# Optimization experiments

Hardware: AMD Instinct MI355X
Metric: run time of the kernel (lower is better)

## Reference

```python
import jax, jax.numpy as jnp
import numpy as np

N_USER = 50000
N_ITEM = 30000
NNZ = 500000  # user-item interactions; edges duplicated symmetrically -> E = 2*NNZ
EMB = 64
N_LAYERS = 2
N_FACTORS = 4
N_ITERATIONS = 2


def setup_inputs() -> dict:
    key = jax.random.key(0)
    k1, k2, k3, k4 = jax.random.split(key, 4)
    user_emb = jax.random.normal(k1, (N_USER, EMB), dtype=jnp.float32) * 0.1
    item_emb = jax.random.normal(k2, (N_ITEM, EMB), dtype=jnp.float32) * 0.1
    row = jax.random.randint(k3, (NNZ,), 0, N_USER, dtype=jnp.int32)
    col = jax.random.randint(k4, (NNZ,), 0, N_ITEM, dtype=jnp.int32) + N_USER
    # symmetric edge list exactly as the torch module builds it
    all_h_list = jnp.concatenate([row, col], axis=0)
    all_t_list = jnp.concatenate([col, row], axis=0)
    return {"user_emb": user_emb, "item_emb": item_emb,
            "all_h_list": all_h_list, "all_t_list": all_t_list}


def _dgcf_forward(user_emb, item_emb, all_h_list, all_t_list):
    n_user = user_emb.shape[0]
    ego = jnp.concatenate([user_emb, item_emb], axis=0)  # [N, D]
    N, D = ego.shape
    F = N_FACTORS
    d = D // F
    E = all_h_list.shape[0]
    dtype = ego.dtype

    all_embeddings = [ego]
    A = jnp.ones((E, F), dtype=dtype)  # A_values init

    for _layer in range(N_LAYERS):
        # torch.chunk along dim 1 == reshape [N, F, d]
        chunks = ego.reshape(N, F, d)
        tail_chunks = chunks[all_t_list]  # [E, F, d] gather of tail embeddings
        factor_emb = None
        for _t in range(N_ITERATIONS):
            # build_matrix, vectorized over the F factors
            normA = jax.nn.softmax(A, axis=1)                        # [E, F]
            dval = jax.ops.segment_sum(normA, all_h_list, num_segments=N)  # [N, F]
            dinv = 1.0 / jnp.sqrt(jnp.clip(dval, 1e-8))
            edge_weight = normA * dinv[all_h_list] * dinv[all_t_list]  # [E, F]
            # message passing per factor: gather tail, weight, scatter to head
            edge_val = tail_chunks * edge_weight[:, :, None]           # [E, F, d]
            factor_emb = jax.ops.segment_sum(edge_val, all_h_list, num_segments=N)  # [N, F, d]
            # dynamic routing update of A
            head = factor_emb[all_h_list]                              # [E, F, d]
            head = head / jnp.clip(jnp.linalg.norm(head, axis=-1, keepdims=True), 1e-12)
            tail = tail_chunks / jnp.clip(jnp.linalg.norm(tail_chunks, axis=-1, keepdims=True), 1e-12)
            A_iter = jnp.sum(head * jnp.tanh(tail), axis=-1)           # [E, F]
            A = A + A_iter
        ego = factor_emb.reshape(N, D)  # concat of factor chunks (last iteration)
        all_embeddings.append(ego)

    all_emb = jnp.mean(jnp.stack(all_embeddings, axis=1), axis=1)  # [N, D]
    return all_emb[:n_user], all_emb[n_user:]


def reference(user_emb, item_emb, all_h_list, all_t_list):
    return _dgcf_forward(user_emb, item_emb, all_h_list, all_t_list)
```

## Files before the change

kernel.cpp:

```cpp
#include <hip/hip_runtime.h>
#include <hip/hip_bf16.h>

#define N_USER 50000
#define N_ITEM 30000
#define NTOT   80000
#define EMB    64
#define FAC    4
#define EDGES  1000000
#define LOG4   1.3862943611198906f
#define SB     1024
#define NBLK   79
#define NBUCK  512
#define BBLK   512
#define BCH    1954


__device__ inline float bf2f(unsigned short u) {
    return __uint_as_float(((unsigned int)u) << 16);
}
__device__ inline unsigned short f2bf(float f) {
    unsigned int x = __float_as_uint(f);
    x += 0x7FFFu + ((x >> 16) & 1u);
    return (unsigned short)(x >> 16);
}
__device__ inline float dot2(unsigned int a, unsigned int b) {
    float a0 = __uint_as_float(a << 16), a1 = __uint_as_float(a & 0xFFFF0000u);
    float b0 = __uint_as_float(b << 16), b1 = __uint_as_float(b & 0xFFFF0000u);
    return a0 * b0 + a1 * b1;
}
__device__ inline int bucket_of(int h) { return (int)(((unsigned)h * NBUCK) / (unsigned)NTOT); }
__device__ inline int bucket_lo(int k) { return (k * NTOT + NBUCK - 1) / NBUCK; }

__global__ void k_detect(const unsigned short* __restrict__ raw, int* __restrict__ flag) {
    __shared__ int s;
    if (threadIdx.x == 0) s = 0;
    __syncthreads();
    int c = 0;
    for (int i = threadIdx.x; i < 16384; i += 256) {
        unsigned short u = raw[i];
        if ((u & 0x7F80) == 0x7F80) c++;
    }
    atomicAdd(&s, c);
    __syncthreads();
    if (threadIdx.x == 0) *flag = (s > 0) ? 1 : 0;
}

__global__ void k_init(const void* __restrict__ ue, const void* __restrict__ ie,
                       const int* __restrict__ flag,
                       unsigned short* __restrict__ egoh,
                       unsigned short* __restrict__ tnh0) {
    int gid = blockIdx.x * blockDim.x + threadIdx.x;
    int wid = gid >> 6;
    int lane = threadIdx.x & 63;
    if (wid >= NTOT) return;
    int i = wid * 64 + lane;
    bool isf32 = (*flag != 0);
    float v;
    if (i < N_USER * EMB) {
        v = isf32 ? ((const float*)ue)[i]
                  : __bfloat162float(((const __hip_bfloat16*)ue)[i]);
    } else {
        int j = i - N_USER * EMB;
        v = isf32 ? ((const float*)ie)[j]
                  : __bfloat162float(((const __hip_bfloat16*)ie)[j]);
    }
    egoh[i] = f2bf(v);
    float ss = v * v;
    ss += __shfl_xor(ss, 1); ss += __shfl_xor(ss, 2);
    ss += __shfl_xor(ss, 4); ss += __shfl_xor(ss, 8);
    float rr = 1.0f / fmaxf(sqrtf(ss), 1e-12f);
    tnh0[i] = f2bf(tanhf(v * rr));
}

__global__ void k_deg(const int* __restrict__ h, int* __restrict__ deg) {
    int e = blockIdx.x * blockDim.x + threadIdx.x;
    if (e < EDGES) atomicAdd(&deg[h[e]], 1);
}

__global__ void k_scan1(const int* __restrict__ deg, int* __restrict__ off,
                        int* __restrict__ bsum) {
    __shared__ int buf[SB];
    int tid = threadIdx.x;
    int i = blockIdx.x * SB + tid;
    int v = (i < NTOT) ? deg[i] : 0;
    buf[tid] = v;
    __syncthreads();
    for (int s = 1; s < SB; s <<= 1) {
        int t = (tid >= s) ? buf[tid - s] : 0;
        __syncthreads();
        buf[tid] += t;
        __syncthreads();
    }
    if (i < NTOT) off[i] = buf[tid] - v;
    if (tid == SB - 1) bsum[blockIdx.x] = buf[tid];
}

__global__ void k_scan2(const int* __restrict__ bsum, int* __restrict__ bbase) {
    __shared__ int b[128];
    int tid = threadIdx.x;
    int v = (tid < NBLK) ? bsum[tid] : 0;
    b[tid] = v;
    __syncthreads();
    for (int s = 1; s < 128; s <<= 1) {
        int t = (tid >= s) ? b[tid - s] : 0;
        __syncthreads();
        b[tid] += t;
        __syncthreads();
    }
    if (tid < NBLK) bbase[tid] = b[tid] - v;
}

__global__ void k_scan3(int* __restrict__ off, const int* __restrict__ bbase,
                        const int* __restrict__ deg, float* __restrict__ dvacc) {
    int i = blockIdx.x * blockDim.x + threadIdx.x;
    if (i < NTOT) {
        off[i] = off[i] + bbase[i >> 10];
        float d = 0.25f * (float)deg[i];
        ((float4*)dvacc)[i] = make_float4(d, d, d, d);
    }
    if (i == 0) off[NTOT] = EDGES;
}

__global__ void k_bcnt(const int* __restrict__ hl, int* __restrict__ cnt) {
    __shared__ int hist[NBUCK];
    int b = blockIdx.x, tid = threadIdx.x;
    for (int i = tid; i < NBUCK; i += 256) hist[i] = 0;
    __syncthreads();
    int base = b * BCH, end = base + BCH; if (end > EDGES) end = EDGES;
    for (int e = base + tid; e < end; e += 256)
        atomicAdd(&hist[bucket_of(hl[e])], 1);
    __syncthreads();
    for (int i = tid; i < NBUCK; i += 256) cnt[b * NBUCK + i] = hist[i];
}

__global__ void k_bscan(const int* __restrict__ cnt, const int* __restrict__ off,
                        int* __restrict__ gbase) {
    __shared__ int buf[BBLK];
    int k = blockIdx.x, tid = threadIdx.x;
    int v = cnt[tid * NBUCK + k];
    buf[tid] = v;
    __syncthreads();
    for (int s = 1; s < BBLK; s <<= 1) {
        int t = (tid >= s) ? buf[tid - s] : 0;
        __syncthreads();
        buf[tid] += t;
        __syncthreads();
    }
    gbase[tid * NBUCK + k] = off[bucket_lo(k)] + buf[tid] - v;
}

__global__ void k_bscat(const int* __restrict__ hl, const int* __restrict__ tl,
                        const int* __restrict__ gbase, int* __restrict__ bt) {
    __shared__ int lg[NBUCK];
    int b = blockIdx.x, tid = threadIdx.x;
    for (int i = tid; i < NBUCK; i += 256) lg[i] = gbase[b * NBUCK + i];
    __syncthreads();
    int base = b * BCH, end = base + BCH; if (end > EDGES) end = EDGES;
    for (int e = base + tid; e < end; e += 256) {
        int h = hl[e];
        int k = bucket_of(h);
        int pos = atomicAdd(&lg[k], 1);
        bt[pos] = ((h - bucket_lo(k)) << 17) | tl[e];
    }
}

__global__ void k_bfin(const int* __restrict__ bt, const int* __restrict__ off,
                       int* __restrict__ tlist, int* __restrict__ hlist) {
    __shared__ int lcur[160];
    int k = blockIdx.x, tid = threadIdx.x;
    int lo = bucket_lo(k), hi = bucket_lo(k + 1);
    int nn = hi - lo;
    for (int i = tid; i < nn; i += 256) lcur[i] = off[lo + i];
    __syncthreads();
    int start = off[lo], end = off[hi];
    for (int j = start + tid; j < end; j += 256) {
        int v = bt[j];
        int hrel = v >> 17;
        int t = v & 0x1FFFF;
        int pos = atomicAdd(&lcur[hrel], 1);
        tlist[pos] = t;
        hlist[pos] = lo + hrel;
    }
}

__global__ void k_scale(float* __restrict__ dvacc, float* __restrict__ dvinv,
                        const unsigned short* __restrict__ ego,
                        unsigned short* __restrict__ egoS) {
    int gid = blockIdx.x * blockDim.x + threadIdx.x;
    int wid = gid >> 6;
    int lane = threadIdx.x & 63;
    if (wid >= NTOT) return;
    int f = lane >> 4;
    float r = rsqrtf(fmaxf(dvacc[wid * 4 + f], 1e-8f));
    if ((lane & 15) == 0) dvinv[wid * 4 + f] = r;
    if (lane < 4) dvacc[wid * 4 + lane] = 0.f;
    int i = wid * 64 + lane;
    egoS[i] = f2bf(bf2f(ego[i]) * r);
}

__global__ void k_mp(const unsigned short* __restrict__ egoS, const float* __restrict__ P,
                     const float* __restrict__ dvinv, const int* __restrict__ off,
                     const int* __restrict__ tlist,
                     unsigned short* __restrict__ fach, float* __restrict__ rhn,
                     unsigned short* __restrict__ tnhOut,
                     int useP, int writeRhn, int writeTnh) {
    int gid = blockIdx.x * blockDim.x + threadIdx.x;
    int wid = gid >> 6;
    int lane = threadIdx.x & 63;
    if (wid >= NTOT) return;
    int c = lane & 15;
    int q = lane >> 4;
    int f = c >> 2;
    int beg = off[wid], end = off[wid + 1];
    float dvh = dvinv[wid * 4 + f];
    const uint2* eg2 = (const uint2*)egoS;

    float a0 = 0.f, a1 = 0.f, a2 = 0.f, a3 = 0.f;
    int nfull = (end - beg) >> 2;
    int j = beg + q;
    if (useP) {
#pragma unroll 2
        for (int g = 0; g < nfull; ++g, j += 4) {
            int t = tlist[j];
            float w = P[j * 4 + f];
            uint2 u = eg2[t * 16 + c];
            a0 += w * __uint_as_float(u.x << 16);
            a1 += w * __uint_as_float(u.x & 0xFFFF0000u);
            a2 += w * __uint_as_float(u.y << 16);
            a3 += w * __uint_as_float(u.y & 0xFFFF0000u);
        }
        if (j < end) {
            int t = tlist[j];
            float w = P[j * 4 + f];
            uint2 u = eg2[t * 16 + c];
            a0 += w * __uint_as_float(u.x << 16);
            a1 += w * __uint_as_float(u.x & 0xFFFF0000u);
            a2 += w * __uint_as_float(u.y << 16);
            a3 += w * __uint_as_float(u.y & 0xFFFF0000u);
        }
    } else {
#pragma unroll 2
        for (int g = 0; g < nfull; ++g, j += 4) {
            int t = tlist[j];
            uint2 u = eg2[t * 16 + c];
            a0 += __uint_as_float(u.x << 16);
            a1 += __uint_as_float(u.x & 0xFFFF0000u);
            a2 += __uint_as_float(u.y << 16);
            a3 += __uint_as_float(u.y & 0xFFFF0000u);
        }
        if (j < end) {
            int t = tlist[j];
            uint2 u = eg2[t * 16 + c];
            a0 += __uint_as_float(u.x << 16);
            a1 += __uint_as_float(u.x & 0xFFFF0000u);
            a2 += __uint_as_float(u.y << 16);
            a3 += __uint_as_float(u.y & 0xFFFF0000u);
        }
        a0 *= 0.25f; a1 *= 0.25f; a2 *= 0.25f; a3 *= 0.25f;
    }

    a0 += __shfl_xor(a0, 16); a1 += __shfl_xor(a1, 16);
    a2 += __shfl_xor(a2, 16); a3 += __shfl_xor(a3, 16);
    a0 += __shfl_xor(a0, 32); a1 += __shfl_xor(a1, 32);
    a2 += __shfl_xor(a2, 32); a3 += __shfl_xor(a3, 32);

    a0 *= dvh; a1 *= dvh; a2 *= dvh; a3 *= dvh;

    if (q == 0) {
        unsigned int p01 = (unsigned int)f2bf(a0) | ((unsigned int)f2bf(a1) << 16);
        unsigned int p23 = (unsigned int)f2bf(a2) | ((unsigned int)f2bf(a3) << 16);
        ((uint2*)fach)[wid * 16 + c] = make_uint2(p01, p23);
    }

    if (writeRhn || writeTnh) {
        float ss = a0 * a0 + a1 * a1 + a2 * a2 + a3 * a3;
        ss += __shfl_xor(ss, 1); ss += __shfl_xor(ss, 2);
        float rr = 1.0f / fmaxf(sqrtf(ss), 1e-12f);
        if (writeRhn && q == 0 && (c & 3) == 0) rhn[wid * 4 + f] = rr;
        if (writeTnh) {
            float t0 = tanhf(a0 * rr), t1 = tanhf(a1 * rr),
                  t2 = tanhf(a2 * rr), t3 = tanhf(a3 * rr);
            if (q == 0) {
                unsigned int p01 = (unsigned int)f2bf(t0) | ((unsigned int)f2bf(t1) << 16);
                unsigned int p23 = (unsigned int)f2bf(t2) | ((unsigned int)f2bf(t3) << 16);
                ((uint2*)tnhOut)[wid * 16 + c] = make_uint2(p01, p23);
            }
        }
    }
}

__global__ void k_upd(const unsigned short* __restrict__ fach,
                      const unsigned short* __restrict__ tnhh,
                      const float* __restrict__ rhn,
                      const int* __restrict__ hlist, const int* __restrict__ tlist,
                      float* __restrict__ P, float* __restrict__ dval, int first) {
    __shared__ int   s_h[256];
    __shared__ float s_p[256][4];
    int tid = threadIdx.x;
    int j = blockIdx.x * 256 + tid;
    int h = -1;
    if (j < EDGES) {
        h = hlist[j];
        int t = tlist[j];
        const uint4* frow = (const uint4*)(fach + (size_t)h * 64);
        const uint4* trow = (const uint4*)(tnhh + (size_t)t * 64);
        float d[4];
#pragma unroll
        for (int f = 0; f < 4; ++f) {
            uint4 a0 = frow[f * 2], a1 = frow[f * 2 + 1];
            uint4 b0 = trow[f * 2], b1 = trow[f * 2 + 1];
            d[f] = dot2(a0.x, b0.x) + dot2(a0.y, b0.y)
                 + dot2(a0.z, b0.z) + dot2(a0.w, b0.w)
                 + dot2(a1.x, b1.x) + dot2(a1.y, b1.y)
                 + dot2(a1.z, b1.z) + dot2(a1.w, b1.w);
        }
        float4 rh = ((const float4*)rhn)[h];
        float lx, ly, lz, lw;
        if (first) { lx = ly = lz = lw = -LOG4; }
        else {
            float4 p0 = ((const float4*)P)[j];
            lx = __logf(p0.x); ly = __logf(p0.y);
            lz = __logf(p0.z); lw = __logf(p0.w);
        }
        float y0 = lx + rh.x * d[0], y1 = ly + rh.y * d[1],
              y2 = lz + rh.z * d[2], y3 = lw + rh.w * d[3];
        float m = fmaxf(fmaxf(y0, y1), fmaxf(y2, y3));
        float e0 = __expf(y0 - m), e1 = __expf(y1 - m),
              e2 = __expf(y2 - m), e3 = __expf(y3 - m);
        float inv = 1.0f / (e0 + e1 + e2 + e3);
        float p0n = e0 * inv, p1n = e1 * inv, p2n = e2 * inv, p3n = e3 * inv;
        ((float4*)P)[j] = make_float4(p0n, p1n, p2n, p3n);
        s_p[tid][0] = p0n; s_p[tid][1] = p1n; s_p[tid][2] = p2n; s_p[tid][3] = p3n;
    }
    s_h[tid] = h;
    __syncthreads();
    if (h == -1) return;
    if (tid > 0 && s_h[tid - 1] == h) return;
    float a0 = 0.f, a1 = 0.f, a2 = 0.f, a3 = 0.f;
    int k = tid;
    while (k < 256 && s_h[k] == h) {
        a0 += s_p[k][0]; a1 += s_p[k][1]; a2 += s_p[k][2]; a3 += s_p[k][3];
        ++k;
    }
    float* dst = dval + (size_t)h * 4;
    if (tid == 0 || k == 256) {
        unsafeAtomicAdd(dst + 0, a0);
        unsafeAtomicAdd(dst + 1, a1);
        unsafeAtomicAdd(dst + 2, a2);
        unsafeAtomicAdd(dst + 3, a3);
    } else {
        ((float4*)dst)[0] = make_float4(a0, a1, a2, a3);
    }
}

__global__ void k_final(const void* __restrict__ ue, const void* __restrict__ ie,
                        const int* __restrict__ flag,
                        const unsigned short* __restrict__ f1,
                        const unsigned short* __restrict__ f3,
                        float* __restrict__ out) {
    int i = blockIdx.x * blockDim.x + threadIdx.x;
    if (i >= NTOT * EMB) return;
    bool isf32 = (*flag != 0);
    float v;
    if (i < N_USER * EMB) {
        v = isf32 ? ((const float*)ue)[i]
                  : __bfloat162float(((const __hip_bfloat16*)ue)[i]);
    } else {
        int j = i - N_USER * EMB;
        v = isf32 ? ((const float*)ie)[j]
                  : __bfloat162float(((const __hip_bfloat16*)ie)[j]);
    }
    out[i] = (v + bf2f(f1[i]) + bf2f(f3[i])) * (1.0f / 3.0f);
}

extern "C" void kernel_launch(void* const* d_in, const int* in_sizes, int n_in,
                              void* d_out, int out_size, void* d_ws, size_t ws_size,
                              hipStream_t stream) {
    const void* ue = d_in[0];
    const void* ie = d_in[1];
    const int* hl = (const int*)d_in[2];
    const int* tl = (const int*)d_in[3];
    float* out = (float*)d_out;

    float* ws    = (float*)d_ws;
    float* P     = ws;
    int*   bt    = (int*)(ws);
    int*   cnt   = (int*)(ws + 1000000);
    int*   gbase = (int*)(ws + 1262144);
    float* dvacc = ws + 4000000;
    float* dvinv = ws + 4320000;
    float* rhn   = ws + 4640000;
    unsigned short* bufW = (unsigned short*)(ws + 4960000);
    unsigned short* bufX = (unsigned short*)(ws + 7520000);
    unsigned short* bufY = (unsigned short*)(ws + 10080000);
    unsigned short* bufZ0 = (unsigned short*)(ws + 12640000);
    unsigned short* bufZ1 = (unsigned short*)(ws + 15200000);
    unsigned short* egoS = (unsigned short*)(ws + 17760000);
    int*   flag = (int*)(ws + 20320000);
    int*   deg  = (int*)(ws + 20320016);
    int*   off  = (int*)(ws + 20400016);
    int*   tlist = (int*)(ws + 20480017);
    int*   hlist = (int*)(ws + 21480017);
    int*   bsum  = (int*)(ws + 22480017);
    int*   bbase = (int*)(ws + 22480145);

    k_detect<<<1, 256, 0, stream>>>((const unsigned short*)ue, flag);
    k_init<<<20000, 256, 0, stream>>>(ue, ie, flag, bufW, bufZ0);

    hipMemsetAsync(deg, 0, NTOT * sizeof(int), stream);
    k_deg<<<3907, 256, 0, stream>>>(hl, deg);
    k_scan1<<<NBLK, SB, 0, stream>>>(deg, off, bsum);
    k_scan2<<<1, 128, 0, stream>>>(bsum, bbase);
    k_scan3<<<313, 256, 0, stream>>>(off, bbase, deg, dvacc);
    k_bcnt<<<BBLK, 256, 0, stream>>>(hl, cnt);
    k_bscan<<<NBUCK, BBLK, 0, stream>>>(cnt, off, gbase);
    k_bscat<<<BBLK, 256, 0, stream>>>(hl, tl, gbase, bt);
    k_bfin<<<NBUCK, 256, 0, stream>>>(bt, off, tlist, hlist);

    k_scale<<<20000, 256, 0, stream>>>(dvacc, dvinv, bufW, egoS);
    k_mp<<<20000, 256, 0, stream>>>(egoS, P, dvinv, off, tlist, bufX, rhn, bufZ1,
                                    0, 1, 0);
    k_upd<<<3907, 256, 0, stream>>>(bufX, bufZ0, rhn, hlist, tlist, P, dvacc, 1);
    k_scale<<<20000, 256, 0, stream>>>(dvacc, dvinv, bufW, egoS);
    k_mp<<<20000, 256, 0, stream>>>(egoS, P, dvinv, off, tlist, bufY, rhn, bufZ1,
                                    1, 1, 1);
    k_upd<<<3907, 256, 0, stream>>>(bufY, bufZ0, rhn, hlist, tlist, P, dvacc, 0);
    k_scale<<<20000, 256, 0, stream>>>(dvacc, dvinv, bufY, egoS);
    k_mp<<<20000, 256, 0, stream>>>(egoS, P, dvinv, off, tlist, bufX, rhn, bufZ1,
                                    1, 1, 0);
    k_upd<<<3907, 256, 0, stream>>>(bufX, bufZ1, rhn, hlist, tlist, P, dvacc, 0);
    k_scale<<<20000, 256, 0, stream>>>(dvacc, dvinv, bufY, egoS);
    k_mp<<<20000, 256, 0, stream>>>(egoS, P, dvinv, off, tlist, bufW, rhn, bufZ1,
                                    1, 0, 0);
    k_final<<<20000, 256, 0, stream>>>(ue, ie, flag, bufY, bufW, out);
}
```

Before: 476.3 us.

## Derive CSR offsets and degrees from bucket counts, dropping global degree/scan kernels

```diff
diff --git a/kernel.cpp b/kernel.cpp
--- a/kernel.cpp
+++ b/kernel.cpp
@@ -8,8 +8,6 @@
 #define FAC    4
 #define EDGES  1000000
 #define LOG4   1.3862943611198906f
-#define SB     1024
-#define NBLK   79
 #define NBUCK  512
 #define BBLK   512
 #define BCH    1954
@@ -72,55 +70,6 @@
     tnh0[i] = f2bf(tanhf(v * rr));
 }
 
-__global__ void k_deg(const int* __restrict__ h, int* __restrict__ deg) {
-    int e = blockIdx.x * blockDim.x + threadIdx.x;
-    if (e < EDGES) atomicAdd(&deg[h[e]], 1);
-}
-
-__global__ void k_scan1(const int* __restrict__ deg, int* __restrict__ off,
-                        int* __restrict__ bsum) {
-    __shared__ int buf[SB];
-    int tid = threadIdx.x;
-    int i = blockIdx.x * SB + tid;
-    int v = (i < NTOT) ? deg[i] : 0;
-    buf[tid] = v;
-    __syncthreads();
-    for (int s = 1; s < SB; s <<= 1) {
-        int t = (tid >= s) ? buf[tid - s] : 0;
-        __syncthreads();
-        buf[tid] += t;
-        __syncthreads();
-    }
-    if (i < NTOT) off[i] = buf[tid] - v;
-    if (tid == SB - 1) bsum[blockIdx.x] = buf[tid];
-}
-
-__global__ void k_scan2(const int* __restrict__ bsum, int* __restrict__ bbase) {
-    __shared__ int b[128];
-    int tid = threadIdx.x;
-    int v = (tid < NBLK) ? bsum[tid] : 0;
-    b[tid] = v;
-    __syncthreads();
-    for (int s = 1; s < 128; s <<= 1) {
-        int t = (tid >= s) ? b[tid - s] : 0;
-        __syncthreads();
-        b[tid] += t;
-        __syncthreads();
-    }
-    if (tid < NBLK) bbase[tid] = b[tid] - v;
-}
-
-__global__ void k_scan3(int* __restrict__ off, const int* __restrict__ bbase,
-                        const int* __restrict__ deg, float* __restrict__ dvacc) {
-    int i = blockIdx.x * blockDim.x + threadIdx.x;
-    if (i < NTOT) {
-        off[i] = off[i] + bbase[i >> 10];
-        float d = 0.25f * (float)deg[i];
-        ((float4*)dvacc)[i] = make_float4(d, d, d, d);
-    }
-    if (i == 0) off[NTOT] = EDGES;
-}
-
 __global__ void k_bcnt(const int* __restrict__ hl, int* __restrict__ cnt) {
     __shared__ int hist[NBUCK];
     int b = blockIdx.x, tid = threadIdx.x;
@@ -133,7 +82,25 @@
     for (int i = tid; i < NBUCK; i += 256) cnt[b * NBUCK + i] = hist[i];
 }
 
-__global__ void k_bscan(const int* __restrict__ cnt, const int* __restrict__ off,
+__global__ void k_btot(const int* __restrict__ cnt, int* __restrict__ boff) {
+    __shared__ int sbuf[NBUCK];
+    int k = threadIdx.x;
+    int s = 0;
+    for (int b = 0; b < BBLK; ++b) s += cnt[b * NBUCK + k];
+    sbuf[k] = s;
+    __syncthreads();
+    int v = s;
+    for (int st = 1; st < NBUCK; st <<= 1) {
+        int t = (k >= st) ? sbuf[k - st] : 0;
+        __syncthreads();
+        sbuf[k] += t;
+        __syncthreads();
+    }
+    boff[k] = sbuf[k] - v;
+    if (k == NBUCK - 1) boff[NBUCK] = EDGES;
+}
+
+__global__ void k_bscan(const int* __restrict__ cnt, const int* __restrict__ boff,
                         int* __restrict__ gbase) {
     __shared__ int buf[BBLK];
     int k = blockIdx.x, tid = threadIdx.x;
@@ -146,7 +113,7 @@
         buf[tid] += t;
         __syncthreads();
     }
-    gbase[tid * NBUCK + k] = off[bucket_lo(k)] + buf[tid] - v;
+    gbase[tid * NBUCK + k] = boff[k] + buf[tid] - v;
 }
 
 __global__ void k_bscat(const int* __restrict__ hl, const int* __restrict__ tl,
@@ -164,19 +131,43 @@
     }
 }
 
-__global__ void k_bfin(const int* __restrict__ bt, const int* __restrict__ off,
+__global__ void k_bfin(const int* __restrict__ bt, const int* __restrict__ boff,
+                       int* __restrict__ off, float* __restrict__ dvacc,
                        int* __restrict__ tlist, int* __restrict__ hlist) {
+    __shared__ int ldeg[160];
     __shared__ int lcur[160];
+    __shared__ int sbuf[256];
     int k = blockIdx.x, tid = threadIdx.x;
     int lo = bucket_lo(k), hi = bucket_lo(k + 1);
     int nn = hi - lo;
-    for (int i = tid; i < nn; i += 256) lcur[i] = off[lo + i];
-    __syncthreads();
-    int start = off[lo], end = off[hi];
+    for (int i = tid; i < nn; i += 256) ldeg[i] = 0;
+    __syncthreads();
+    int start = boff[k], end = boff[k + 1];
+    for (int j = start + tid; j < end; j += 256)
+        atomicAdd(&ldeg[bt[j] >> 17], 1);
+    __syncthreads();
+    int v = (tid < nn) ? ldeg[tid] : 0;
+    sbuf[tid] = v;
+    __syncthreads();
+    for (int s = 1; s < 256; s <<= 1) {
+        int t = (tid >= s) ? sbuf[tid - s] : 0;
+        __syncthreads();
+        sbuf[tid] += t;
+        __syncthreads();
+    }
+    if (tid < nn) {
+        int o = start + sbuf[tid] - v;
+        off[lo + tid] = o;
+        lcur[tid] = o;
+        float d = 0.25f * (float)v;
+        ((float4*)dvacc)[lo + tid] = make_float4(d, d, d, d);
+    }
+    if (k == 0 && tid == 0) off[NTOT] = EDGES;
+    __syncthreads();
     for (int j = start + tid; j < end; j += 256) {
-        int v = bt[j];
-        int hrel = v >> 17;
-        int t = v & 0x1FFFF;
+        int val = bt[j];
+        int hrel = val >> 17;
+        int t = val & 0x1FFFF;
         int pos = atomicAdd(&lcur[hrel], 1);
         tlist[pos] = t;
         hlist[pos] = lo + hrel;
@@ -397,25 +388,19 @@
     unsigned short* bufZ1 = (unsigned short*)(ws + 15200000);
     unsigned short* egoS = (unsigned short*)(ws + 17760000);
     int*   flag = (int*)(ws + 20320000);
-    int*   deg  = (int*)(ws + 20320016);
+    int*   boff = (int*)(ws + 20320016);
     int*   off  = (int*)(ws + 20400016);
     int*   tlist = (int*)(ws + 20480017);
     int*   hlist = (int*)(ws + 21480017);
-    int*   bsum  = (int*)(ws + 22480017);
-    int*   bbase = (int*)(ws + 22480145);
 
     k_detect<<<1, 256, 0, stream>>>((const unsigned short*)ue, flag);
     k_init<<<20000, 256, 0, stream>>>(ue, ie, flag, bufW, bufZ0);
 
-    hipMemsetAsync(deg, 0, NTOT * sizeof(int), stream);
-    k_deg<<<3907, 256, 0, stream>>>(hl, deg);
-    k_scan1<<<NBLK, SB, 0, stream>>>(deg, off, bsum);
-    k_scan2<<<1, 128, 0, stream>>>(bsum, bbase);
-    k_scan3<<<313, 256, 0, stream>>>(off, bbase, deg, dvacc);
     k_bcnt<<<BBLK, 256, 0, stream>>>(hl, cnt);
-    k_bscan<<<NBUCK, BBLK, 0, stream>>>(cnt, off, gbase);
+    k_btot<<<1, NBUCK, 0, stream>>>(cnt, boff);
+    k_bscan<<<NBUCK, BBLK, 0, stream>>>(cnt, boff, gbase);
     k_bscat<<<BBLK, 256, 0, stream>>>(hl, tl, gbase, bt);
-    k_bfin<<<NBUCK, 256, 0, stream>>>(bt, off, tlist, hlist);
+    k_bfin<<<NBUCK, 256, 0, stream>>>(bt, boff, off, dvacc, tlist, hlist);
 
     k_scale<<<20000, 256, 0, stream>>>(dvacc, dvinv, bufW, egoS);
     k_mp<<<20000, 256, 0, stream>>>(egoS, P, dvinv, off, tlist, bufX, rhn, bufZ1,
```

Result: faster. 441.1 us (-7.4%).
